# Kernel optimization log

Hardware: AMD Instinct MI355X
Metric: run time of the kernel (lower is better)

The kernel has to match this reference:

```python
import jax, jax.numpy as jnp
import numpy as np

N_NODES = 50000
N_EDGES = 800000
N_HIDDEN = 64
N_LAYER = 3
IN_DIM = 4


def setup_inputs() -> dict:
    key = jax.random.key(0)
    ks = jax.random.split(key, 10)
    x = jax.random.normal(ks[0], (N_NODES, IN_DIM), dtype=jnp.float32)
    edge_index = jax.random.randint(ks[1], (2, N_EDGES), 0, N_NODES, dtype=jnp.int64)
    # Glorot-style params matching pyg GCNConv (lin has no bias; conv adds bias after aggregation)
    def glorot(k, fan_in, fan_out):
        s = jnp.sqrt(6.0 / (fan_in + fan_out))
        return jax.random.uniform(k, (fan_in, fan_out), jnp.float32, -s, s)
    W_in = glorot(ks[2], IN_DIM, N_HIDDEN)
    b_in = jnp.zeros((N_HIDDEN,), jnp.float32)
    W_h = jnp.stack([glorot(jax.random.fold_in(ks[3], i), N_HIDDEN, N_HIDDEN) for i in range(N_LAYER)])
    b_h = jnp.zeros((N_LAYER, N_HIDDEN), jnp.float32)
    W_out = glorot(ks[4], N_HIDDEN, 1)
    b_out = jnp.zeros((1,), jnp.float32)
    return {"x": x, "edge_index": edge_index, "W_in": W_in, "b_in": b_in,
            "W_h": W_h, "b_h": b_h, "W_out": W_out, "b_out": b_out}


def _gcn_norm(edge_index, n_nodes):
    # add self-loops, compute symmetric norm D^{-1/2} (A+I) D^{-1/2}
    loop = jnp.arange(n_nodes, dtype=edge_index.dtype)
    src = jnp.concatenate([edge_index[0], loop])
    dst = jnp.concatenate([edge_index[1], loop])
    deg = jax.ops.segment_sum(jnp.ones_like(dst, dtype=jnp.float32), dst, num_segments=n_nodes)
    dinv = jax.lax.rsqrt(deg)  # deg >= 1 due to self-loops
    norm = dinv[src] * dinv[dst]
    return src, dst, norm


def _gcn_conv(x, W, b, src, dst, norm, n_nodes):
    h = x @ W                                   # [N, out]
    msg = h[src] * norm[:, None]                # gather + scale, [E+N, out]
    out = jax.ops.segment_sum(msg, dst, num_segments=n_nodes)  # scatter-add
    return out + b


def reference(x, edge_index, W_in, b_in, W_h, b_h, W_out, b_out):
    n = x.shape[0]
    src, dst, norm = _gcn_norm(edge_index, n)
    h = jax.nn.relu(_gcn_conv(x, W_in, b_in, src, dst, norm, n))
    for i in range(W_h.shape[0]):
        h = jax.nn.relu(_gcn_conv(h, W_h[i], b_h[i], src, dst, norm, n))
    return _gcn_conv(h, W_out, b_out, src, dst, norm, n)
```

## Files before the change

### kernel.cpp

```cpp
#include <hip/hip_runtime.h>
#include <hip/hip_bf16.h>


#define TPB 256
typedef __hip_bfloat16 bf16;
#define B2F __bfloat162float

__global__ void k_zero_cnt(int* __restrict__ cnt, int n) {
    int i = blockIdx.x * blockDim.x + threadIdx.x;
    if (i < n) cnt[i] = 0;
}

__global__ void k_hist(const int* __restrict__ dst, int* __restrict__ cnt, int E, int n) {
    int e = blockIdx.x * blockDim.x + threadIdx.x;
    if (e < E) {
        int d = dst[e];
        if ((unsigned)d < (unsigned)n) atomicAdd(&cnt[d], 1);
    }
}

__global__ void k_blocksum(const int* __restrict__ cnt, int* __restrict__ bsum, int n) {
    __shared__ int s[TPB];
    int i = blockIdx.x * TPB + threadIdx.x;
    s[threadIdx.x] = (i < n) ? cnt[i] : 0;
    __syncthreads();
    for (int off = TPB / 2; off > 0; off >>= 1) {
        if (threadIdx.x < off) s[threadIdx.x] += s[threadIdx.x + off];
        __syncthreads();
    }
    if (threadIdx.x == 0) bsum[blockIdx.x] = s[0];
}

__global__ void k_scan_bsum(int* __restrict__ bsum, int nb) {
    __shared__ int s[TPB];
    int t = threadIdx.x;
    int v = (t < nb) ? bsum[t] : 0;
    s[t] = v;
    __syncthreads();
    for (int off = 1; off < TPB; off <<= 1) {
        int u = (t >= off) ? s[t - off] : 0;
        __syncthreads();
        s[t] += u;
        __syncthreads();
    }
    if (t < nb) bsum[t] = s[t] - v;
}

__global__ void k_scan_final(const int* __restrict__ cnt, const int* __restrict__ bsum,
                             int* __restrict__ row_start, int* __restrict__ cursor,
                             float* __restrict__ dinv, int n) {
    __shared__ int s[TPB];
    int t = threadIdx.x;
    int i = blockIdx.x * TPB + t;
    int v = (i < n) ? cnt[i] : 0;
    s[t] = v;
    __syncthreads();
    for (int off = 1; off < TPB; off <<= 1) {
        int u = (t >= off) ? s[t - off] : 0;
        __syncthreads();
        s[t] += u;
        __syncthreads();
    }
    if (i < n) {
        int excl = bsum[blockIdx.x] + s[t] - v;
        row_start[i] = excl;
        cursor[i] = excl;
        dinv[i] = rsqrtf((float)v + 1.0f);
        if (i == n - 1) row_start[n] = excl + v;
    }
}

__global__ void k_scatter(const int* __restrict__ src, const int* __restrict__ dst,
                          int* __restrict__ cursor, unsigned short* __restrict__ bucket,
                          int E, int n) {
    int e = blockIdx.x * blockDim.x + threadIdx.x;
    if (e < E) {
        int d = dst[e], s = src[e];
        if ((unsigned)d >= (unsigned)n || (unsigned)s >= (unsigned)n) return;
        int pos = atomicAdd(&cursor[d], 1);
        if ((unsigned)pos < (unsigned)E) bucket[pos] = (unsigned short)s;
    }
}

__global__ void k_mm_in(const float* __restrict__ x, const float* __restrict__ W,
                        const float* __restrict__ dinv, bf16* __restrict__ g, int n) {
    int t = blockIdx.x * blockDim.x + threadIdx.x;
    if (t >= n * 64) return;
    int i = t >> 6, j = t & 63;
    float acc = 0.f;
#pragma unroll
    for (int k = 0; k < 4; ++k) acc = fmaf(x[i * 4 + k], W[k * 64 + j], acc);
    g[t] = __float2bfloat16(acc * dinv[i]);
}

__device__ __forceinline__ void acc_quad(float4& a, uint2 w) {
    a.x += __uint_as_float(w.x << 16);
    a.y += __uint_as_float(w.x & 0xffff0000u);
    a.z += __uint_as_float(w.y << 16);
    a.w += __uint_as_float(w.y & 0xffff0000u);
}

__device__ __forceinline__ void agg_row_quad(const bf16* __restrict__ g,
                                             const unsigned short* __restrict__ bucket,
                                             int k0, int k1, int d, float* __restrict__ sVrow,
                                             int lane, unsigned nm1, unsigned Em1) {
    int grp = lane >> 4, i = lane & 15;
    float4 a = {0.f, 0.f, 0.f, 0.f};
    if (grp == 0) {
        uint2 w = *(const uint2*)(g + (size_t)d * 64 + 4 * i);
        acc_quad(a, w);
    }
    for (int base = k0; base < k1; base += 64) {
        int cnt = min(64, k1 - base);
        int rec = bucket[min((unsigned)(base + lane), Em1)];
        int k = 0;
        for (; k + 16 <= cnt; k += 16) {
            unsigned s0 = min((unsigned)__shfl(rec, k + 0 + grp), nm1);
            unsigned s1 = min((unsigned)__shfl(rec, k + 4 + grp), nm1);
            unsigned s2 = min((unsigned)__shfl(rec, k + 8 + grp), nm1);
            unsigned s3 = min((unsigned)__shfl(rec, k + 12 + grp), nm1);
            uint2 w0 = *(const uint2*)(g + (size_t)s0 * 64 + 4 * i);
            uint2 w1 = *(const uint2*)(g + (size_t)s1 * 64 + 4 * i);
            uint2 w2 = *(const uint2*)(g + (size_t)s2 * 64 + 4 * i);
            uint2 w3 = *(const uint2*)(g + (size_t)s3 * 64 + 4 * i);
            acc_quad(a, w0); acc_quad(a, w1); acc_quad(a, w2); acc_quad(a, w3);
        }
        for (; k < cnt; k += 4) {
            int e = k + grp;
            unsigned s = min((unsigned)__shfl(rec, min(e, 63)), nm1);
            uint2 w = *(const uint2*)(g + (size_t)s * 64 + 4 * i);
            if (e < cnt) acc_quad(a, w);
        }
    }
#pragma unroll
    for (int m = 16; m < 64; m <<= 1) {
        a.x += __shfl_xor(a.x, m);
        a.y += __shfl_xor(a.y, m);
        a.z += __shfl_xor(a.z, m);
        a.w += __shfl_xor(a.w, m);
    }
    if (grp == 0) ((float4*)sVrow)[i] = a;
}

__global__ __launch_bounds__(TPB) void k_gconv(
    const bf16* __restrict__ gIn, const float* __restrict__ dinv,
    const int* __restrict__ row_start, const unsigned short* __restrict__ bucket,
    const float* __restrict__ bias, const float* __restrict__ W,
    bf16* __restrict__ gOut, int n, int E) {
    __shared__ float sW[64 * 64];
    __shared__ float sV[4][64];
    int tid = threadIdx.x;
    for (int k = tid; k < 1024; k += TPB) ((float4*)sW)[k] = ((const float4*)W)[k];
    int r = tid >> 6, j = tid & 63;
    int d = blockIdx.x * 4 + r;
    float dd = 0.f;
    if (d < n) {
        dd = dinv[d];
        int k0 = row_start[d], k1 = row_start[d + 1];
        k1 = min(k1, E); k0 = max(min(k0, k1), 0);
        agg_row_quad(gIn, bucket, k0, k1, d, sV[r], j, (unsigned)(n - 1), (unsigned)(E - 1));
    }
    __syncthreads();
    if (d < n) sV[r][j] = fmaxf(fmaf(dd, sV[r][j], bias[j]), 0.f);
    __syncthreads();
    if (d >= n) return;
    float acc = 0.f;
#pragma unroll
    for (int k = 0; k < 64; ++k) acc = fmaf(sV[r][k], sW[k * 64 + j], acc);
    gOut[(size_t)d * 64 + j] = __float2bfloat16(acc * dd);
}

__global__ __launch_bounds__(TPB) void k_gconv_z(
    const bf16* __restrict__ gIn, const float* __restrict__ dinv,
    const int* __restrict__ row_start, const unsigned short* __restrict__ bucket,
    const float* __restrict__ bias, const float* __restrict__ Wout,
    float* __restrict__ zg, int n, int E) {
    __shared__ float sV[4][64];
    int tid = threadIdx.x;
    int r = tid >> 6, j = tid & 63;
    int d = blockIdx.x * 4 + r;
    if (d >= n) return;
    float dd = dinv[d];
    int k0 = row_start[d], k1 = row_start[d + 1];
    k1 = min(k1, E); k0 = max(min(k0, k1), 0);
    agg_row_quad(gIn, bucket, k0, k1, d, sV[r], j, (unsigned)(n - 1), (unsigned)(E - 1));
    __syncthreads();
    float v = fmaxf(fmaf(dd, sV[r][j], bias[j]), 0.f) * Wout[j];
#pragma unroll
    for (int off = 32; off > 0; off >>= 1) v += __shfl_down(v, off);
    if (j == 0) zg[d] = v * dd;
}

__global__ __launch_bounds__(TPB) void k_out(
    const float* __restrict__ zg, const float* __restrict__ dinv,
    const int* __restrict__ row_start, const unsigned short* __restrict__ bucket,
    const float* __restrict__ b_out, float* __restrict__ out, int n, int E) {
    int t = blockIdx.x * blockDim.x + threadIdx.x;
    int d = t >> 6, lane = t & 63;
    if (d >= n) return;
    int k0 = row_start[d], k1 = row_start[d + 1];
    k1 = min(k1, E); k0 = max(min(k0, k1), 0);
    unsigned nm1 = (unsigned)(n - 1);
    float v = 0.f;
    for (int k = k0 + lane; k < k1; k += 64) {
        unsigned s = min((unsigned)bucket[k], nm1);
        v += zg[s];
    }
#pragma unroll
    for (int off = 32; off > 0; off >>= 1) v += __shfl_down(v, off);
    if (lane == 0) out[d] = fmaf(zg[d] + v, dinv[d], b_out[0]);
}

extern "C" void kernel_launch(void* const* d_in, const int* in_sizes, int n_in,
                              void* d_out, int out_size, void* d_ws, size_t ws_size,
                              hipStream_t stream) {
    const float* x     = (const float*)d_in[0];
    const int*   ei    = (const int*)d_in[1];
    const float* W_in  = (const float*)d_in[2];
    const float* b_in  = (const float*)d_in[3];
    const float* W_h   = (const float*)d_in[4];
    const float* b_h   = (const float*)d_in[5];
    const float* W_out = (const float*)d_in[6];
    const float* b_out = (const float*)d_in[7];
    float* out = (float*)d_out;

    int N = in_sizes[0] / 4;
    int E = in_sizes[1] / 2;
    const int* src = ei;
    const int* dst = ei + E;

    char* ws = (char*)d_ws;
    bf16* gA              = (bf16*)ws;           ws += (size_t)N * 64 * 2;
    bf16* gB              = (bf16*)ws;           ws += (size_t)N * 64 * 2;
    unsigned short* bucket = (unsigned short*)ws; ws += (size_t)E * 2;
    int*  row_start       = (int*)ws;            ws += (size_t)(N + 1) * 4;
    int*  cursor          = (int*)ws;            ws += (size_t)N * 4;
    int*  cnt             = (int*)ws;            ws += (size_t)N * 4;
    float* dinv           = (float*)ws;          ws += (size_t)N * 4;
    float* zg             = (float*)ws;          ws += (size_t)N * 4;
    int*  bsum            = (int*)ws;

    int gN  = (N + TPB - 1) / TPB;
    int gE  = (E + TPB - 1) / TPB;
    int gNF = (N * 64 + TPB - 1) / TPB;
    int gN4 = (N + 3) / 4;

    k_zero_cnt<<<gN, TPB, 0, stream>>>(cnt, N);
    k_hist<<<gE, TPB, 0, stream>>>(dst, cnt, E, N);
    k_blocksum<<<gN, TPB, 0, stream>>>(cnt, bsum, N);
    k_scan_bsum<<<1, TPB, 0, stream>>>(bsum, gN);
    k_scan_final<<<gN, TPB, 0, stream>>>(cnt, bsum, row_start, cursor, dinv, N);
    k_scatter<<<gE, TPB, 0, stream>>>(src, dst, cursor, bucket, E, N);

    k_mm_in<<<gNF, TPB, 0, stream>>>(x, W_in, dinv, gA, N);
    k_gconv<<<gN4, TPB, 0, stream>>>(gA, dinv, row_start, bucket, b_in, W_h, gB, N, E);
    k_gconv<<<gN4, TPB, 0, stream>>>(gB, dinv, row_start, bucket, b_h, W_h + 4096, gA, N, E);
    k_gconv<<<gN4, TPB, 0, stream>>>(gA, dinv, row_start, bucket, b_h + 64, W_h + 8192, gB, N, E);
    k_gconv_z<<<gN4, TPB, 0, stream>>>(gB, dinv, row_start, bucket, b_h + 128, W_out, zg, N, E);
    k_out<<<gN4, TPB, 0, stream>>>(zg, dinv, row_start, bucket, b_out, out, N, E);
}
```

Measured before the change: 316.8 us.

## Replace global edge scatter with two-pass block-binned CSR build

The single global-atomic scatter that builds the CSR bucket is replaced by a two-pass scheme. Edges are first binned into 256-node ranges using shared-memory histograms and one global atomic per bin per block, then each bin is scattered locally so the cursor atomics and bucket writes hit a compact region. The aggregation also drops the cross-group shuffle reduction and has each group write its partial sum to shared memory, summing them afterwards. The matvec reads activations as float4. This adds a staging buffer of E words and two extra launches. It assumes there are at most 256 bins (N up to 65536), which matches the existing 16-bit index limit.

```diff
diff --git a/kernel.cpp b/kernel.cpp
--- a/kernel.cpp
+++ b/kernel.cpp
@@ -3,6 +3,8 @@
 
 
 #define TPB 256
+#define EPT 8
+#define CHUNK (TPB * EPT)
 typedef __hip_bfloat16 bf16;
 #define B2F __bfloat162float
 
@@ -70,15 +72,64 @@
     }
 }
 
-__global__ void k_scatter(const int* __restrict__ src, const int* __restrict__ dst,
-                          int* __restrict__ cursor, unsigned short* __restrict__ bucket,
-                          int E, int n) {
-    int e = blockIdx.x * blockDim.x + threadIdx.x;
-    if (e < E) {
-        int d = dst[e], s = src[e];
-        if ((unsigned)d >= (unsigned)n || (unsigned)s >= (unsigned)n) return;
+__global__ void k_init_bcur(const int* __restrict__ row_start, int* __restrict__ bcur,
+                            int B, int n) {
+    int b = threadIdx.x;
+    if (b < B) bcur[b] = row_start[min(b << 8, n)];
+}
+
+__global__ __launch_bounds__(TPB) void k_bin(
+    const int* __restrict__ src, const int* __restrict__ dst,
+    int* __restrict__ bcur, unsigned* __restrict__ staging, int E, int n) {
+    __shared__ int hcnt[256];
+    __shared__ int hbase[256];
+    int tid = threadIdx.x;
+    int e0 = blockIdx.x * CHUNK;
+    hcnt[tid] = 0;
+    __syncthreads();
+
+    int eb[EPT];
+    unsigned rec[EPT];
+#pragma unroll
+    for (int u = 0; u < EPT; ++u) {
+        int e = e0 + u * TPB + tid;
+        eb[u] = -1;
+        if (e < E) {
+            int d = dst[e], s = src[e];
+            if ((unsigned)d < (unsigned)n && (unsigned)s < (unsigned)n) {
+                eb[u] = d >> 8;
+                rec[u] = (unsigned)s | ((unsigned)(d & 255) << 16);
+                atomicAdd(&hcnt[eb[u]], 1);
+            }
+        }
+    }
+    __syncthreads();
+    int c = hcnt[tid];
+    hbase[tid] = (c > 0) ? atomicAdd(&bcur[tid], c) : 0;
+    hcnt[tid] = 0;
+    __syncthreads();
+#pragma unroll
+    for (int u = 0; u < EPT; ++u) {
+        if (eb[u] >= 0) {
+            int r = atomicAdd(&hcnt[eb[u]], 1);
+            int pos = hbase[eb[u]] + r;
+            if ((unsigned)pos < (unsigned)E) staging[pos] = rec[u];
+        }
+    }
+}
+
+__global__ __launch_bounds__(TPB) void k_unbin(
+    const unsigned* __restrict__ staging, const int* __restrict__ row_start,
+    int* __restrict__ cursor, unsigned short* __restrict__ bucket, int E, int n) {
+    int b = blockIdx.x;
+    int lo = row_start[min(b << 8, n)];
+    int hi = row_start[min((b + 1) << 8, n)];
+    lo = max(0, min(lo, E)); hi = max(lo, min(hi, E));
+    for (int i = lo + threadIdx.x; i < hi; i += TPB) {
+        unsigned r = staging[i];
+        int d = min((b << 8) + (int)(r >> 16), n - 1);
         int pos = atomicAdd(&cursor[d], 1);
-        if ((unsigned)pos < (unsigned)E) bucket[pos] = (unsigned short)s;
+        if ((unsigned)pos < (unsigned)E) bucket[pos] = (unsigned short)(r & 0xffffu);
     }
 }
 
@@ -102,7 +153,7 @@
 
 __device__ __forceinline__ void agg_row_quad(const bf16* __restrict__ g,
                                              const unsigned short* __restrict__ bucket,
-                                             int k0, int k1, int d, float* __restrict__ sVrow,
+                                             int k0, int k1, int d, float* __restrict__ sVp,
                                              int lane, unsigned nm1, unsigned Em1) {
     int grp = lane >> 4, i = lane & 15;
     float4 a = {0.f, 0.f, 0.f, 0.f};
@@ -132,14 +183,7 @@
             if (e < cnt) acc_quad(a, w);
         }
     }
-#pragma unroll
-    for (int m = 16; m < 64; m <<= 1) {
-        a.x += __shfl_xor(a.x, m);
-        a.y += __shfl_xor(a.y, m);
-        a.z += __shfl_xor(a.z, m);
-        a.w += __shfl_xor(a.w, m);
-    }
-    if (grp == 0) ((float4*)sVrow)[i] = a;
+    ((float4*)(sVp + grp * 64))[i] = a;
 }
 
 __global__ __launch_bounds__(TPB) void k_gconv(
@@ -148,7 +192,7 @@
     const float* __restrict__ bias, const float* __restrict__ W,
     bf16* __restrict__ gOut, int n, int E) {
     __shared__ float sW[64 * 64];
-    __shared__ float sV[4][64];
+    __shared__ float sVp[4][4 * 64];
     int tid = threadIdx.x;
     for (int k = tid; k < 1024; k += TPB) ((float4*)sW)[k] = ((const float4*)W)[k];
     int r = tid >> 6, j = tid & 63;
@@ -158,15 +202,24 @@
         dd = dinv[d];
         int k0 = row_start[d], k1 = row_start[d + 1];
         k1 = min(k1, E); k0 = max(min(k0, k1), 0);
-        agg_row_quad(gIn, bucket, k0, k1, d, sV[r], j, (unsigned)(n - 1), (unsigned)(E - 1));
-    }
-    __syncthreads();
-    if (d < n) sV[r][j] = fmaxf(fmaf(dd, sV[r][j], bias[j]), 0.f);
+        agg_row_quad(gIn, bucket, k0, k1, d, sVp[r], j, (unsigned)(n - 1), (unsigned)(E - 1));
+    }
+    __syncthreads();
+    float v = sVp[r][j] + sVp[r][64 + j] + sVp[r][128 + j] + sVp[r][192 + j];
+    float a = fmaxf(fmaf(dd, v, bias[j]), 0.f);
+    if (d < n) sVp[r][j] = a;
     __syncthreads();
     if (d >= n) return;
+    const float4* ap = (const float4*)&sVp[r][0];
     float acc = 0.f;
 #pragma unroll
-    for (int k = 0; k < 64; ++k) acc = fmaf(sV[r][k], sW[k * 64 + j], acc);
+    for (int k4 = 0; k4 < 16; ++k4) {
+        float4 a4 = ap[k4];
+        acc = fmaf(a4.x, sW[(4 * k4 + 0) * 64 + j], acc);
+        acc = fmaf(a4.y, sW[(4 * k4 + 1) * 64 + j], acc);
+        acc = fmaf(a4.z, sW[(4 * k4 + 2) * 64 + j], acc);
+        acc = fmaf(a4.w, sW[(4 * k4 + 3) * 64 + j], acc);
+    }
     gOut[(size_t)d * 64 + j] = __float2bfloat16(acc * dd);
 }
 
@@ -175,20 +228,24 @@
     const int* __restrict__ row_start, const unsigned short* __restrict__ bucket,
     const float* __restrict__ bias, const float* __restrict__ Wout,
     float* __restrict__ zg, int n, int E) {
-    __shared__ float sV[4][64];
+    __shared__ float sVp[4][4 * 64];
     int tid = threadIdx.x;
     int r = tid >> 6, j = tid & 63;
     int d = blockIdx.x * 4 + r;
+    float dd = 0.f;
+    if (d < n) {
+        dd = dinv[d];
+        int k0 = row_start[d], k1 = row_start[d + 1];
+        k1 = min(k1, E); k0 = max(min(k0, k1), 0);
+        agg_row_quad(gIn, bucket, k0, k1, d, sVp[r], j, (unsigned)(n - 1), (unsigned)(E - 1));
+    }
+    __syncthreads();
     if (d >= n) return;
-    float dd = dinv[d];
-    int k0 = row_start[d], k1 = row_start[d + 1];
-    k1 = min(k1, E); k0 = max(min(k0, k1), 0);
-    agg_row_quad(gIn, bucket, k0, k1, d, sV[r], j, (unsigned)(n - 1), (unsigned)(E - 1));
-    __syncthreads();
-    float v = fmaxf(fmaf(dd, sV[r][j], bias[j]), 0.f) * Wout[j];
-#pragma unroll
-    for (int off = 32; off > 0; off >>= 1) v += __shfl_down(v, off);
-    if (j == 0) zg[d] = v * dd;
+    float v = sVp[r][j] + sVp[r][64 + j] + sVp[r][128 + j] + sVp[r][192 + j];
+    float a = fmaxf(fmaf(dd, v, bias[j]), 0.f) * Wout[j];
+#pragma unroll
+    for (int off = 32; off > 0; off >>= 1) a += __shfl_down(a, off);
+    if (j == 0) zg[d] = a * dd;
 }
 
 __global__ __launch_bounds__(TPB) void k_out(
@@ -230,27 +287,33 @@
     const int* dst = ei + E;
 
     char* ws = (char*)d_ws;
-    bf16* gA              = (bf16*)ws;           ws += (size_t)N * 64 * 2;
-    bf16* gB              = (bf16*)ws;           ws += (size_t)N * 64 * 2;
+    bf16* gA               = (bf16*)ws;           ws += (size_t)N * 64 * 2;
+    bf16* gB               = (bf16*)ws;           ws += (size_t)N * 64 * 2;
     unsigned short* bucket = (unsigned short*)ws; ws += (size_t)E * 2;
-    int*  row_start       = (int*)ws;            ws += (size_t)(N + 1) * 4;
-    int*  cursor          = (int*)ws;            ws += (size_t)N * 4;
-    int*  cnt             = (int*)ws;            ws += (size_t)N * 4;
-    float* dinv           = (float*)ws;          ws += (size_t)N * 4;
-    float* zg             = (float*)ws;          ws += (size_t)N * 4;
-    int*  bsum            = (int*)ws;
-
+    unsigned* staging      = (unsigned*)ws;       ws += (size_t)E * 4;
+    int*  row_start        = (int*)ws;            ws += (size_t)(N + 1) * 4;
+    int*  cursor           = (int*)ws;            ws += (size_t)N * 4;
+    int*  cnt              = (int*)ws;            ws += (size_t)N * 4;
+    float* dinv            = (float*)ws;          ws += (size_t)N * 4;
+    float* zg              = (float*)ws;          ws += (size_t)N * 4;
+    int*  bsum             = (int*)ws;            ws += 257 * 4;
+    int*  bcur             = (int*)ws;
+
+    int B   = (N + 255) >> 8;
     int gN  = (N + TPB - 1) / TPB;
     int gE  = (E + TPB - 1) / TPB;
     int gNF = (N * 64 + TPB - 1) / TPB;
     int gN4 = (N + 3) / 4;
+    int gBin = (E + CHUNK - 1) / CHUNK;
 
     k_zero_cnt<<<gN, TPB, 0, stream>>>(cnt, N);
     k_hist<<<gE, TPB, 0, stream>>>(dst, cnt, E, N);
     k_blocksum<<<gN, TPB, 0, stream>>>(cnt, bsum, N);
     k_scan_bsum<<<1, TPB, 0, stream>>>(bsum, gN);
     k_scan_final<<<gN, TPB, 0, stream>>>(cnt, bsum, row_start, cursor, dinv, N);
-    k_scatter<<<gE, TPB, 0, stream>>>(src, dst, cursor, bucket, E, N);
+    k_init_bcur<<<1, TPB, 0, stream>>>(row_start, bcur, B, N);
+    k_bin<<<gBin, TPB, 0, stream>>>(src, dst, bcur, staging, E, N);
+    k_unbin<<<B, TPB, 0, stream>>>(staging, row_start, cursor, bucket, E, N);
 
     k_mm_in<<<gNF, TPB, 0, stream>>>(x, W_in, dinv, gA, N);
     k_gconv<<<gN4, TPB, 0, stream>>>(gA, dinv, row_start, bucket, b_in, W_h, gB, N, E);
```

Measured after the change: 310.5 us. 1.02x faster.
